# Kernel tuning notes

Measured on AMD Instinct MI355X. Metric: run time of the kernel, lower is better.

## Reference

```python
import jax, jax.numpy as jnp
import numpy as np

B, N, K = 4, 40960, 16
D_IN, D_OUT = 32, 64


def setup_inputs() -> dict:
    key = jax.random.key(0)
    keys = iter(jax.random.split(key, 48))
    def nrm(shape, scale):
        return (jax.random.normal(next(keys), shape, jnp.float32) * scale).astype(jnp.float32)
    inp = {
        "feature": jax.random.normal(next(keys), (B, N, D_IN), jnp.float32),
        "xyz": jax.random.uniform(next(keys), (B, N, 3), jnp.float32),
        "neigh_idx": jax.random.randint(next(keys), (B, N, K), 0, N, jnp.int32),
    }
    def conv_bn(name, cin, cout):
        inp["w_" + name] = nrm((cin, cout), (2.0 / cin) ** 0.5)
        inp["s_" + name] = 1.0 + nrm((cout,), 0.1)  # folded BN scale: gamma/sqrt(var+eps)
        inp["b_" + name] = nrm((cout,), 0.1)        # folded BN bias: beta - mean*scale
    conv_bn("mlp1", D_IN, D_OUT // 2)
    conv_bn("lfa1", 10, D_OUT // 2)
    inp["w_att1_fc"] = nrm((D_OUT, D_OUT), (2.0 / D_OUT) ** 0.5)
    conv_bn("att1_mlp", D_OUT, D_OUT // 2)
    conv_bn("lfa2", D_OUT // 2, D_OUT // 2)
    inp["w_att2_fc"] = nrm((D_OUT, D_OUT), (2.0 / D_OUT) ** 0.5)
    conv_bn("att2_mlp", D_OUT, D_OUT)
    conv_bn("mlp2", D_OUT, 2 * D_OUT)
    conv_bn("sc", D_IN, 2 * D_OUT)
    return inp


def _gather(pc, idx):
    # pc: [B,N,D], idx: [B,N,K] -> [B,N,K,D]
    b, n, k = idx.shape
    flat = jnp.take_along_axis(pc, idx.reshape(b, n * k, 1), axis=1)
    return flat.reshape(b, n, k, pc.shape[-1])


def _cb(x, w, s, b, relu=True):
    # 1x1 conv + folded BN (+ ReLU), channels-last
    y = jnp.einsum('...i,io->...o', x, w) * s + b
    return jnp.maximum(y, 0.0) if relu else y


def _att_pool(fs, w_fc, w, s, b):
    # fs: [B,N,K,C]; softmax-attention pooling over K, then mlp
    scores = jax.nn.softmax(jnp.einsum('bnkc,cd->bnkd', fs, w_fc), axis=2)
    agg = jnp.sum(fs * scores, axis=2)  # [B,N,C]
    return _cb(agg, w, s, b)


def _rel_pos(xyz, idx):
    nbr = _gather(xyz, idx)                           # [B,N,K,3]
    tile = jnp.broadcast_to(xyz[:, :, None, :], nbr.shape)
    rel = tile - nbr
    dist = jnp.sqrt(jnp.sum(rel * rel, axis=-1, keepdims=True))
    return jnp.concatenate([dist, rel, tile, nbr], axis=-1)  # [B,N,K,10]


def reference(feature, xyz, neigh_idx,
              w_mlp1, s_mlp1, b_mlp1,
              w_lfa1, s_lfa1, b_lfa1,
              w_att1_fc, w_att1_mlp, s_att1_mlp, b_att1_mlp,
              w_lfa2, s_lfa2, b_lfa2,
              w_att2_fc, w_att2_mlp, s_att2_mlp, b_att2_mlp,
              w_mlp2, s_mlp2, b_mlp2,
              w_sc, s_sc, b_sc):
    f_pc = _cb(feature, w_mlp1, s_mlp1, b_mlp1)                   # [B,N,d/2]
    f_xyz = _cb(_rel_pos(xyz, neigh_idx), w_lfa1, s_lfa1, b_lfa1)  # [B,N,K,d/2]
    f_nb = _gather(f_pc, neigh_idx)                                # [B,N,K,d/2]
    f_agg = _att_pool(jnp.concatenate([f_nb, f_xyz], axis=-1),
                      w_att1_fc, w_att1_mlp, s_att1_mlp, b_att1_mlp)  # [B,N,d/2]
    f_xyz2 = _cb(f_xyz, w_lfa2, s_lfa2, b_lfa2)                    # [B,N,K,d/2]
    f_nb2 = _gather(f_agg, neigh_idx)                              # [B,N,K,d/2]
    f_pc2 = _att_pool(jnp.concatenate([f_nb2, f_xyz2], axis=-1),
                      w_att2_fc, w_att2_mlp, s_att2_mlp, b_att2_mlp)  # [B,N,d]
    out = _cb(f_pc2, w_mlp2, s_mlp2, b_mlp2, relu=False)           # [B,N,2d]
    sc = _cb(feature, w_sc, s_sc, b_sc, relu=False)
    return jax.nn.leaky_relu(out + sc, negative_slope=0.2)
```

## Files before the change

kernel.cpp:

```cpp
#include <hip/hip_runtime.h>
#include <hip/hip_bf16.h>

#define NPTS  40960
#define BNPTS 163840
#define KNB   16

#define PK_MLP1 0
#define PK_FC1  1280
#define PK_FC2  6912
#define PK_L1   12544
#define PK_L2   13824
#define PK_M1   15104
#define PK_M2   17920
#define PK_W2   23552
#define PK_WS   34816
#define PK_TOTAL 39936

using bf16x8 = __attribute__((ext_vector_type(8))) short;
using f32x4  = __attribute__((ext_vector_type(4))) float;

__device__ __forceinline__ unsigned short f2bf(float x) {
    union { float f; unsigned u; } v; v.f = x;
    unsigned r = v.u + 0x7fffu + ((v.u >> 16) & 1u);
    return (unsigned short)(r >> 16);
}
__device__ __forceinline__ float bf2f(unsigned short u) {
    union { unsigned u; float f; } v; v.u = ((unsigned)u) << 16;
    return v.f;
}
__device__ __forceinline__ unsigned pk2(float lo, float hi) {
    union { __hip_bfloat162 h; unsigned u; } v;
    v.h = __float22bfloat162_rn(float2{lo, hi});
    return v.u;
}
__device__ __forceinline__ bf16x8 pack8(float a0, float a1, float a2, float a3,
                                        float a4, float a5, float a6, float a7) {
    union { unsigned u[4]; bf16x8 v; } w;
    w.u[0] = pk2(a0, a1); w.u[1] = pk2(a2, a3);
    w.u[2] = pk2(a4, a5); w.u[3] = pk2(a6, a7);
    return w.v;
}
__device__ __forceinline__ f32x4 mfma16(bf16x8 a, bf16x8 b, f32x4 c) {
    return __builtin_amdgcn_mfma_f32_16x16x32_bf16(a, b, c, 0, 0, 0);
}
__device__ __forceinline__ float exp2_fast(float x) { return __builtin_amdgcn_exp2f(x); }
__device__ __forceinline__ float rcp_fast(float x)  { return __builtin_amdgcn_rcpf(x); }

__global__ __launch_bounds__(256)
void k_prep(const float* __restrict__ wm1, const float* __restrict__ wfc1,
            const float* __restrict__ wfc2,
            const float* __restrict__ wlfa1, const float* __restrict__ slfa1, const float* __restrict__ blfa1,
            const float* __restrict__ wlfa2,
            const float* __restrict__ wam1, const float* __restrict__ wam2,
            const float* __restrict__ w2, const float* __restrict__ wsc,
            unsigned short* __restrict__ pk)
{
    const int tid = threadIdx.x, blk = blockIdx.x;
    const float LOG2E = 1.4426950408889634f;
    switch (blk) {
    case 0:
        for (int t = tid; t < 32 * 32; t += 256) {
            int c = t >> 5, d = t & 31;
            int slot = (d & 1) * 16 + (d >> 1);
            pk[PK_MLP1 + slot * 40 + c] = f2bf(wm1[t]);
        }
        break;
    case 1:
        for (int t = tid; t < 64 * 64; t += 256) {
            int c = t >> 6, d = t & 63;
            pk[PK_FC1 + d * 88 + c] = f2bf(wfc1[t] * LOG2E);
        }
        break;
    case 2:
        for (int t = tid; t < 64 * 64; t += 256) {
            int c = t >> 6, d = t & 63;
            pk[PK_FC2 + d * 88 + c] = f2bf(wfc2[t] * LOG2E);
        }
        break;
    case 3:
        for (int t = tid; t < 32 * 32; t += 256) {
            int k = t >> 5, d = t & 31;
            int slot = (d & 1) * 16 + (d >> 1);
            float v1 = k < 10 ? wlfa1[k * 32 + d] * slfa1[d] : (k == 10 ? blfa1[d] : 0.f);
            pk[PK_L1 + slot * 40 + k] = f2bf(v1);
            pk[PK_L2 + slot * 40 + k] = f2bf(wlfa2[k * 32 + d]);
        }
        break;
    case 4:
        for (int t = tid; t < 64 * 32; t += 256) {
            int c = t / 32, d = t % 32;
            int slot = (d & 1) * 16 + (d >> 1);
            pk[PK_M1 + slot * 88 + c] = f2bf(wam1[t]);
        }
        break;
    case 5:
        for (int t = tid; t < 64 * 64; t += 256) {
            int c = t >> 6, d = t & 63;
            int slot = (d >> 5) * 32 + (d & 1) * 16 + ((d & 31) >> 1);
            pk[PK_M2 + slot * 88 + c] = f2bf(wam2[t]);
        }
        break;
    case 6:
        for (int t = tid; t < 64 * 128; t += 256) {
            int c = t >> 7, d = t & 127;
            int slot = (d >> 5) * 32 + (d & 1) * 16 + ((d & 31) >> 1);
            pk[PK_W2 + slot * 88 + c] = f2bf(w2[t]);
        }
        break;
    case 7:
        for (int t = tid; t < 32 * 128; t += 256) {
            int c = t >> 7, d = t & 127;
            int slot = (d >> 5) * 32 + (d & 1) * 16 + ((d & 31) >> 1);
            pk[PK_WS + slot * 40 + c] = f2bf(wsc[t]);
        }
        break;
    }
}

__global__ __launch_bounds__(256)
void k_mlp1(const float* __restrict__ feature, const unsigned short* __restrict__ pk,
            const float* __restrict__ s, const float* __restrict__ b,
            unsigned short* __restrict__ f_pc)
{
    const int tid = threadIdx.x;
    const int lid = tid & 63, wv = tid >> 6;
    const int col = lid & 15, quad = lid >> 4;
    bf16x8 B0 = *(const bf16x8*)&pk[PK_MLP1 + col * 40 + quad * 8];
    bf16x8 B1 = *(const bf16x8*)&pk[PK_MLP1 + (16 + col) * 40 + quad * 8];
    float s0 = s[2 * col], b0 = b[2 * col], s1 = s[2 * col + 1], b1 = b[2 * col + 1];
    for (int itp = 0; itp < 4; itp++) {
        const int p0 = blockIdx.x * 256 + wv * 64 + itp * 16;
        const float* fr = &feature[(size_t)(p0 + col) * 32 + quad * 8];
        float4 u0 = *(const float4*)fr;
        float4 u1 = *(const float4*)(fr + 4);
        bf16x8 a = pack8(u0.x, u0.y, u0.z, u0.w, u1.x, u1.y, u1.z, u1.w);
        f32x4 z = {0.f, 0.f, 0.f, 0.f};
        f32x4 d0 = mfma16(a, B0, z);
        f32x4 d1 = mfma16(a, B1, z);
        #pragma unroll
        for (int r = 0; r < 4; r++) {
            int p = p0 + quad * 4 + r;
            float ye = fmaxf(d0[r] * s0 + b0, 0.f);
            float yo = fmaxf(d1[r] * s1 + b1, 0.f);
            *(unsigned*)&f_pc[(size_t)p * 32 + 2 * col] = pk2(ye, yo);
        }
    }
}

template<int NOUT, bool HAS_LFA2>
__global__ __launch_bounds__(256, 4)
void k_att(const float* __restrict__ xyz, const int* __restrict__ nidx,
           const unsigned short* __restrict__ src,
           const unsigned short* __restrict__ wl1T, const unsigned short* __restrict__ wl2T,
           const float* __restrict__ slfa2, const float* __restrict__ blfa2,
           const unsigned short* __restrict__ wfcT, const unsigned short* __restrict__ wmT,
           const float* __restrict__ smlp, const float* __restrict__ bmlp,
           unsigned short* __restrict__ out)
{
    constexpr int NP = NOUT / 32;
    constexpr int WS = 88;
    __shared__ __align__(16) char smem[27648];
    char* uni = smem;

    const int tid = threadIdx.x;
    const int lid = tid & 63, wv = tid >> 6;
    const int col = lid & 15, quad = lid >> 4;

    bf16x8 Bfc[4][2];
    #pragma unroll
    for (int nt = 0; nt < 4; nt++)
        #pragma unroll
        for (int ks = 0; ks < 2; ks++)
            Bfc[nt][ks] = *(const bf16x8*)&wfcT[(nt * 16 + col) * WS + ks * 32 + quad * 8];
    bf16x8 Bl1e = *(const bf16x8*)&wl1T[col * 40 + quad * 8];
    bf16x8 Bl1o = *(const bf16x8*)&wl1T[(16 + col) * 40 + quad * 8];
    bf16x8 Bl2e{}, Bl2o{};
    float sl2e = 0.f, bl2e = 0.f, sl2o = 0.f, bl2o = 0.f;
    if (HAS_LFA2) {
        Bl2e = *(const bf16x8*)&wl2T[col * 40 + quad * 8];
        Bl2o = *(const bf16x8*)&wl2T[(16 + col) * 40 + quad * 8];
        sl2e = slfa2[2 * col]; bl2e = blfa2[2 * col];
        sl2o = slfa2[2 * col + 1]; bl2o = blfa2[2 * col + 1];
    }
    float sme[NP], bme[NP], smo[NP], bmo[NP];
    #pragma unroll
    for (int tp = 0; tp < NP; tp++) {
        sme[tp] = smlp[tp * 32 + 2 * col]; bme[tp] = bmlp[tp * 32 + 2 * col];
        smo[tp] = smlp[tp * 32 + 2 * col + 1]; bmo[tp] = bmlp[tp * 32 + 2 * col + 1];
    }
    bf16x8 Bme_r[2], Bmo_r[2];
    if constexpr (NOUT == 32) {
        #pragma unroll
        for (int ks = 0; ks < 2; ks++) {
            Bme_r[ks] = *(const bf16x8*)&wmT[col * WS + ks * 32 + quad * 8];
            Bmo_r[ks] = *(const bf16x8*)&wmT[(16 + col) * WS + ks * 32 + quad * 8];
        }
    }

    unsigned short* fc  = (unsigned short*)(uni) + wv * 2816;
    unsigned short* ag  = (unsigned short*)(uni + 22528) + wv * 288;
    unsigned short* nb  = (unsigned short*)(uni + 24832) + wv * 256;
    float*          cxy = (float*)(uni + 26880) + wv * 48;

    const int blk = (int)blockIdx.x;
    const int vblk = (blk & 7) * 320 + (blk >> 3);
    const int pbase = vblk * 64 + wv * 16;
    const int pb = (pbase / NPTS) * NPTS;
    const unsigned short* srcb = src + (size_t)pb * 32;
    const float* xyzb = xyz + (size_t)pb * 3;

    {
        int4 t4 = *(const int4*)&nidx[(size_t)pbase * KNB + lid * 4];
        ushort4 u = make_ushort4((unsigned short)t4.x, (unsigned short)t4.y,
                                 (unsigned short)t4.z, (unsigned short)t4.w);
        *(ushort4*)&nb[lid * 4] = u;
        if (lid < 48) cxy[lid] = xyz[(size_t)pbase * 3 + lid];
    }

    const f32x4 z = {0.f, 0.f, 0.f, 0.f};
    bf16x8 vs; float nx = 0.f, ny = 0.f, nz = 0.f;
    {
        int j = (int)nb[col];
        vs = *(const bf16x8*)(srcb + (size_t)j * 32 + quad * 8);
        if (quad < 2) { const float* xp = xyzb + (size_t)j * 3; nx = xp[0]; ny = xp[1]; nz = xp[2]; }
    }

    #pragma unroll 2
    for (int it = 0; it < 16; it++) {
        const int p = pbase + it;
        unsigned short* fcb = fc + (it & 1) * 1408;
        bf16x8 a0 = vs;
        *(bf16x8*)&fcb[col * WS + quad * 8] = a0;

        float cx = cxy[it * 3], cy = cxy[it * 3 + 1], cz = cxy[it * 3 + 2];
        float rx = cx - nx, ry = cy - ny, rz = cz - nz;
        float dd = sqrtf(rx * rx + ry * ry + rz * rz);
        float f0 = 0.f, f1 = 0.f, f2 = 0.f, f3 = 0.f, f4 = 0.f, f5 = 0.f, f6 = 0.f, f7 = 0.f;
        if (quad == 0)      { f0 = dd; f1 = rx; f2 = ry; f3 = rz; f4 = cx; f5 = cy; f6 = cz; f7 = nx; }
        else if (quad == 1) { f0 = ny; f1 = nz; f2 = 1.0f; }
        bf16x8 al = pack8(f0, f1, f2, f3, f4, f5, f6, f7);

        {
            int itn = it < 15 ? it + 1 : 15;
            int j = (int)nb[itn * 16 + col];
            vs = *(const bf16x8*)(srcb + (size_t)j * 32 + quad * 8);
            if (quad < 2) { const float* xp = xyzb + (size_t)j * 3; nx = xp[0]; ny = xp[1]; nz = xp[2]; }
        }

        {
            f32x4 d0 = mfma16(al, Bl1e, z);
            f32x4 d1 = mfma16(al, Bl1o, z);
            #pragma unroll
            for (int r = 0; r < 4; r++) {
                float ye = fmaxf(d0[r], 0.f);
                float yo = fmaxf(d1[r], 0.f);
                *(unsigned*)&fcb[(quad * 4 + r) * WS + 32 + 2 * col] = pk2(ye, yo);
            }
            if (HAS_LFA2) {
                bf16x8 a2 = *(const bf16x8*)&fcb[col * WS + 32 + quad * 8];
                f32x4 e0 = mfma16(a2, Bl2e, z);
                f32x4 e1 = mfma16(a2, Bl2o, z);
                #pragma unroll
                for (int r = 0; r < 4; r++) {
                    float ye = fmaxf(e0[r] * sl2e + bl2e, 0.f);
                    float yo = fmaxf(e1[r] * sl2o + bl2o, 0.f);
                    *(unsigned*)&fcb[(quad * 4 + r) * WS + 32 + 2 * col] = pk2(ye, yo);
                }
            }
        }

        {
            bf16x8 a1 = *(const bf16x8*)&fcb[col * WS + 32 + quad * 8];
            #pragma unroll
            for (int nt = 0; nt < 4; nt++) {
                f32x4 L = mfma16(a1, Bfc[nt][1], mfma16(a0, Bfc[nt][0], z));
                float e0 = exp2_fast(L[0]), e1 = exp2_fast(L[1]);
                float e2 = exp2_fast(L[2]), e3 = exp2_fast(L[3]);
                float sden = (e0 + e1) + (e2 + e3);
                const unsigned short* frr = &fcb[quad * 4 * WS + nt * 16 + col];
                float av = e0 * bf2f(frr[0]) + e1 * bf2f(frr[WS]) + e2 * bf2f(frr[2 * WS]) + e3 * bf2f(frr[3 * WS]);
                av   += __shfl_xor(av, 16, 64);
                sden += __shfl_xor(sden, 16, 64);
                av   += __shfl_xor(av, 32, 64);
                sden += __shfl_xor(sden, 32, 64);
                if (quad == 0) ag[(it & 3) * 72 + nt * 16 + col] = f2bf(av * rcp_fast(sden));
            }
        }

        if ((it & 3) == 3) {
            bf16x8 am0 = *(const bf16x8*)&ag[(col & 3) * 72 + quad * 8];
            bf16x8 am1 = *(const bf16x8*)&ag[(col & 3) * 72 + 32 + quad * 8];
            #pragma unroll
            for (int tp = 0; tp < NP; tp++) {
                bf16x8 Be0, Be1, Bo0, Bo1;
                if constexpr (NOUT == 32) {
                    Be0 = Bme_r[0]; Be1 = Bme_r[1];
                    Bo0 = Bmo_r[0]; Bo1 = Bmo_r[1];
                } else {
                    Be0 = *(const bf16x8*)&wmT[(tp * 32 + col) * WS + quad * 8];
                    Be1 = *(const bf16x8*)&wmT[(tp * 32 + col) * WS + 32 + quad * 8];
                    Bo0 = *(const bf16x8*)&wmT[(tp * 32 + 16 + col) * WS + quad * 8];
                    Bo1 = *(const bf16x8*)&wmT[(tp * 32 + 16 + col) * WS + 32 + quad * 8];
                }
                f32x4 de = mfma16(am1, Be1, mfma16(am0, Be0, z));
                f32x4 dq = mfma16(am1, Bo1, mfma16(am0, Bo0, z));
                if (quad == 0) {
                    #pragma unroll
                    for (int r = 0; r < 4; r++) {
                        float ye = fmaxf(de[r] * sme[tp] + bme[tp], 0.f);
                        float yo = fmaxf(dq[r] * smo[tp] + bmo[tp], 0.f);
                        *(unsigned*)&out[(size_t)(p - 3 + r) * NOUT + tp * 32 + 2 * col] = pk2(ye, yo);
                    }
                }
            }
        }
    }
}

__global__ __launch_bounds__(256)
void k_out(const unsigned short* __restrict__ f_pc2, const float* __restrict__ feature,
           const unsigned short* __restrict__ pk,
           const float* __restrict__ s2, const float* __restrict__ b2,
           const float* __restrict__ ssc, const float* __restrict__ bsc,
           float* __restrict__ out)
{
    const int tid = threadIdx.x;
    const int lid = tid & 63, wv = tid >> 6;
    const int col = lid & 15, quad = lid >> 4;
    const unsigned short* w2T = pk + PK_W2;
    const unsigned short* wsT = pk + PK_WS;
    float sse[4], sso[4], ste[4], sto[4], bbe[4], bbo[4];
    #pragma unroll
    for (int m = 0; m < 4; m++) {
        int ce = m * 32 + 2 * col, co = ce + 1;
        sse[m] = s2[ce]; sso[m] = s2[co];
        ste[m] = ssc[ce]; sto[m] = ssc[co];
        bbe[m] = b2[ce] + bsc[ce]; bbo[m] = b2[co] + bsc[co];
    }
    const f32x4 z = {0.f, 0.f, 0.f, 0.f};
    #pragma unroll 1
    for (int itp = 0; itp < 2; itp++) {
        const int p0 = blockIdx.x * 128 + wv * 32 + itp * 16;
        const unsigned short* ar = &f_pc2[(size_t)(p0 + col) * 64 + quad * 8];
        bf16x8 a10 = *(const bf16x8*)ar;
        bf16x8 a11 = *(const bf16x8*)(ar + 32);
        const float* fr = &feature[(size_t)(p0 + col) * 32 + quad * 8];
        float4 u0 = *(const float4*)fr;
        float4 u1 = *(const float4*)(fr + 4);
        bf16x8 a2 = pack8(u0.x, u0.y, u0.z, u0.w, u1.x, u1.y, u1.z, u1.w);
        #pragma unroll
        for (int m = 0; m < 4; m++) {
            bf16x8 ke0 = *(const bf16x8*)&w2T[(m * 32 + col) * 88 + quad * 8];
            bf16x8 ke1 = *(const bf16x8*)&w2T[(m * 32 + col) * 88 + 32 + quad * 8];
            bf16x8 ko0 = *(const bf16x8*)&w2T[(m * 32 + 16 + col) * 88 + quad * 8];
            bf16x8 ko1 = *(const bf16x8*)&w2T[(m * 32 + 16 + col) * 88 + 32 + quad * 8];
            bf16x8 se  = *(const bf16x8*)&wsT[(m * 32 + col) * 40 + quad * 8];
            bf16x8 so  = *(const bf16x8*)&wsT[(m * 32 + 16 + col) * 40 + quad * 8];
            f32x4 de = mfma16(a11, ke1, mfma16(a10, ke0, z));
            f32x4 dq = mfma16(a11, ko1, mfma16(a10, ko0, z));
            f32x4 ee = mfma16(a2, se, z);
            f32x4 eo = mfma16(a2, so, z);
            #pragma unroll
            for (int r = 0; r < 4; r++) {
                float ye = de[r] * sse[m] + ee[r] * ste[m] + bbe[m];
                float yo = dq[r] * sso[m] + eo[r] * sto[m] + bbo[m];
                ye = ye > 0.f ? ye : 0.2f * ye;
                yo = yo > 0.f ? yo : 0.2f * yo;
                *(float2*)&out[(size_t)(p0 + quad * 4 + r) * 128 + m * 32 + 2 * col] =
                    make_float2(ye, yo);
            }
        }
    }
}

extern "C" void kernel_launch(void* const* d_in, const int* in_sizes, int n_in,
                              void* d_out, int out_size, void* d_ws, size_t ws_size,
                              hipStream_t stream) {
    const float* feature = (const float*)d_in[0];
    const float* xyz     = (const float*)d_in[1];
    const int*   nidx    = (const int*)d_in[2];
    const float* w_mlp1 = (const float*)d_in[3];
    const float* s_mlp1 = (const float*)d_in[4];
    const float* b_mlp1 = (const float*)d_in[5];
    const float* w_lfa1 = (const float*)d_in[6];
    const float* s_lfa1 = (const float*)d_in[7];
    const float* b_lfa1 = (const float*)d_in[8];
    const float* w_att1_fc  = (const float*)d_in[9];
    const float* w_att1_mlp = (const float*)d_in[10];
    const float* s_att1_mlp = (const float*)d_in[11];
    const float* b_att1_mlp = (const float*)d_in[12];
    const float* w_lfa2 = (const float*)d_in[13];
    const float* s_lfa2 = (const float*)d_in[14];
    const float* b_lfa2 = (const float*)d_in[15];
    const float* w_att2_fc  = (const float*)d_in[16];
    const float* w_att2_mlp = (const float*)d_in[17];
    const float* s_att2_mlp = (const float*)d_in[18];
    const float* b_att2_mlp = (const float*)d_in[19];
    const float* w_mlp2 = (const float*)d_in[20];
    const float* s_mlp2 = (const float*)d_in[21];
    const float* b_mlp2 = (const float*)d_in[22];
    const float* w_sc = (const float*)d_in[23];
    const float* s_sc = (const float*)d_in[24];
    const float* b_sc = (const float*)d_in[25];

    unsigned short* f_pc  = (unsigned short*)d_ws;
    unsigned short* f_agg = f_pc  + (size_t)BNPTS * 32;
    unsigned short* f_pc2 = f_agg + (size_t)BNPTS * 32;
    unsigned short* pkw   = f_pc2 + (size_t)BNPTS * 64;
    float* out = (float*)d_out;

    k_prep<<<8, 256, 0, stream>>>(w_mlp1, w_att1_fc, w_att2_fc,
                                  w_lfa1, s_lfa1, b_lfa1, w_lfa2,
                                  w_att1_mlp, w_att2_mlp, w_mlp2, w_sc, pkw);
    k_mlp1<<<BNPTS / 256, 256, 0, stream>>>(feature, pkw, s_mlp1, b_mlp1, f_pc);
    k_att<32, false><<<BNPTS / 64, 256, 0, stream>>>(
        xyz, nidx, f_pc,
        pkw + PK_L1, pkw + PK_L1,
        s_lfa1, b_lfa1,
        pkw + PK_FC1, pkw + PK_M1, s_att1_mlp, b_att1_mlp, f_agg);
    k_att<64, true><<<BNPTS / 64, 256, 0, stream>>>(
        xyz, nidx, f_agg,
        pkw + PK_L1, pkw + PK_L2,
        s_lfa2, b_lfa2,
        pkw + PK_FC2, pkw + PK_M2, s_att2_mlp, b_att2_mlp, f_pc2);
    k_out<<<BNPTS / 128, 256, 0, stream>>>(
        f_pc2, feature, pkw,
        s_mlp2, b_mlp2, s_sc, b_sc, out);
}
```

Before: 365.5 us.

## Pad xyz to float4 for gathers and batch attention-MLP epilogue per wave

Adds a prep pass that repacks xyz into a padded float4 array, so each neighbor coordinate gather in the attention kernels becomes a single 16-byte load instead of three scalar loads. The attention kernels also drop the double-buffered feature tile and the every-4-points MLP epilogue. They now collect all 16 aggregated rows in shared memory and run one 16-row MFMA epilogue per wave, with all lanes storing output. This reduces shared memory and per-iteration branching, at the cost of extra xyz4 workspace, an extra prep pass, and a fully serial loop (unroll 1) with less overlap across iterations.

```diff
diff --git a/kernel.cpp b/kernel.cpp
--- a/kernel.cpp
+++ b/kernel.cpp
@@ -53,10 +53,17 @@
             const float* __restrict__ wlfa2,
             const float* __restrict__ wam1, const float* __restrict__ wam2,
             const float* __restrict__ w2, const float* __restrict__ wsc,
-            unsigned short* __restrict__ pk)
+            const float* __restrict__ xyz,
+            unsigned short* __restrict__ pk, float* __restrict__ xyz4)
 {
     const int tid = threadIdx.x, blk = blockIdx.x;
     const float LOG2E = 1.4426950408889634f;
+    if (blk >= 8) {
+        int idx = (blk - 8) * 256 + tid;
+        float3 v = *(const float3*)&xyz[(size_t)idx * 3];
+        *(float4*)&xyz4[(size_t)idx * 4] = make_float4(v.x, v.y, v.z, 0.f);
+        return;
+    }
     switch (blk) {
     case 0:
         for (int t = tid; t < 32 * 32; t += 256) {
@@ -149,7 +156,7 @@
 
 template<int NOUT, bool HAS_LFA2>
 __global__ __launch_bounds__(256, 4)
-void k_att(const float* __restrict__ xyz, const int* __restrict__ nidx,
+void k_att(const float* __restrict__ xyz4, const int* __restrict__ nidx,
            const unsigned short* __restrict__ src,
            const unsigned short* __restrict__ wl1T, const unsigned short* __restrict__ wl2T,
            const float* __restrict__ slfa2, const float* __restrict__ blfa2,
@@ -159,7 +166,7 @@
 {
     constexpr int NP = NOUT / 32;
     constexpr int WS = 88;
-    __shared__ __align__(16) char smem[27648];
+    __shared__ __align__(16) char smem[23552];
     char* uni = smem;
 
     const int tid = threadIdx.x;
@@ -188,33 +195,26 @@
         sme[tp] = smlp[tp * 32 + 2 * col]; bme[tp] = bmlp[tp * 32 + 2 * col];
         smo[tp] = smlp[tp * 32 + 2 * col + 1]; bmo[tp] = bmlp[tp * 32 + 2 * col + 1];
     }
-    bf16x8 Bme_r[2], Bmo_r[2];
-    if constexpr (NOUT == 32) {
-        #pragma unroll
-        for (int ks = 0; ks < 2; ks++) {
-            Bme_r[ks] = *(const bf16x8*)&wmT[col * WS + ks * 32 + quad * 8];
-            Bmo_r[ks] = *(const bf16x8*)&wmT[(16 + col) * WS + ks * 32 + quad * 8];
-        }
-    }
-
-    unsigned short* fc  = (unsigned short*)(uni) + wv * 2816;
-    unsigned short* ag  = (unsigned short*)(uni + 22528) + wv * 288;
-    unsigned short* nb  = (unsigned short*)(uni + 24832) + wv * 256;
-    float*          cxy = (float*)(uni + 26880) + wv * 48;
+
+    unsigned short* fc  = (unsigned short*)(uni) + wv * 1408;
+    unsigned short* ag  = (unsigned short*)(uni + 11264) + wv * 1152;
+    unsigned short* nb  = (unsigned short*)(uni + 20480) + wv * 256;
+    float*          cxy = (float*)(uni + 22528) + wv * 64;
 
     const int blk = (int)blockIdx.x;
     const int vblk = (blk & 7) * 320 + (blk >> 3);
     const int pbase = vblk * 64 + wv * 16;
     const int pb = (pbase / NPTS) * NPTS;
     const unsigned short* srcb = src + (size_t)pb * 32;
-    const float* xyzb = xyz + (size_t)pb * 3;
+    const float4* x4  = (const float4*)xyz4;
+    const float4* x4b = x4 + pb;
 
     {
         int4 t4 = *(const int4*)&nidx[(size_t)pbase * KNB + lid * 4];
         ushort4 u = make_ushort4((unsigned short)t4.x, (unsigned short)t4.y,
                                  (unsigned short)t4.z, (unsigned short)t4.w);
         *(ushort4*)&nb[lid * 4] = u;
-        if (lid < 48) cxy[lid] = xyz[(size_t)pbase * 3 + lid];
+        if (lid < 16) *(float4*)&cxy[lid * 4] = x4[pbase + lid];
     }
 
     const f32x4 z = {0.f, 0.f, 0.f, 0.f};
@@ -222,17 +222,15 @@
     {
         int j = (int)nb[col];
         vs = *(const bf16x8*)(srcb + (size_t)j * 32 + quad * 8);
-        if (quad < 2) { const float* xp = xyzb + (size_t)j * 3; nx = xp[0]; ny = xp[1]; nz = xp[2]; }
-    }
-
-    #pragma unroll 2
+        if (quad < 2) { float4 t = x4b[j]; nx = t.x; ny = t.y; nz = t.z; }
+    }
+
+    #pragma unroll 1
     for (int it = 0; it < 16; it++) {
-        const int p = pbase + it;
-        unsigned short* fcb = fc + (it & 1) * 1408;
         bf16x8 a0 = vs;
-        *(bf16x8*)&fcb[col * WS + quad * 8] = a0;
-
-        float cx = cxy[it * 3], cy = cxy[it * 3 + 1], cz = cxy[it * 3 + 2];
+        *(bf16x8*)&fc[col * WS + quad * 8] = a0;
+
+        float cx = cxy[it * 4], cy = cxy[it * 4 + 1], cz = cxy[it * 4 + 2];
         float rx = cx - nx, ry = cy - ny, rz = cz - nz;
         float dd = sqrtf(rx * rx + ry * ry + rz * rz);
         float f0 = 0.f, f1 = 0.f, f2 = 0.f, f3 = 0.f, f4 = 0.f, f5 = 0.f, f6 = 0.f, f7 = 0.f;
@@ -244,7 +242,7 @@
             int itn = it < 15 ? it + 1 : 15;
             int j = (int)nb[itn * 16 + col];
             vs = *(const bf16x8*)(srcb + (size_t)j * 32 + quad * 8);
-            if (quad < 2) { const float* xp = xyzb + (size_t)j * 3; nx = xp[0]; ny = xp[1]; nz = xp[2]; }
+            if (quad < 2) { float4 t = x4b[j]; nx = t.x; ny = t.y; nz = t.z; }
         }
 
         {
@@ -254,64 +252,65 @@
             for (int r = 0; r < 4; r++) {
                 float ye = fmaxf(d0[r], 0.f);
                 float yo = fmaxf(d1[r], 0.f);
-                *(unsigned*)&fcb[(quad * 4 + r) * WS + 32 + 2 * col] = pk2(ye, yo);
+                *(unsigned*)&fc[(quad * 4 + r) * WS + 32 + 2 * col] = pk2(ye, yo);
             }
             if (HAS_LFA2) {
-                bf16x8 a2 = *(const bf16x8*)&fcb[col * WS + 32 + quad * 8];
+                bf16x8 a2 = *(const bf16x8*)&fc[col * WS + 32 + quad * 8];
                 f32x4 e0 = mfma16(a2, Bl2e, z);
                 f32x4 e1 = mfma16(a2, Bl2o, z);
                 #pragma unroll
                 for (int r = 0; r < 4; r++) {
                     float ye = fmaxf(e0[r] * sl2e + bl2e, 0.f);
                     float yo = fmaxf(e1[r] * sl2o + bl2o, 0.f);
-                    *(unsigned*)&fcb[(quad * 4 + r) * WS + 32 + 2 * col] = pk2(ye, yo);
+                    *(unsigned*)&fc[(quad * 4 + r) * WS + 32 + 2 * col] = pk2(ye, yo);
                 }
             }
         }
 
         {
-            bf16x8 a1 = *(const bf16x8*)&fcb[col * WS + 32 + quad * 8];
+            bf16x8 a1 = *(const bf16x8*)&fc[col * WS + 32 + quad * 8];
             #pragma unroll
             for (int nt = 0; nt < 4; nt++) {
                 f32x4 L = mfma16(a1, Bfc[nt][1], mfma16(a0, Bfc[nt][0], z));
                 float e0 = exp2_fast(L[0]), e1 = exp2_fast(L[1]);
                 float e2 = exp2_fast(L[2]), e3 = exp2_fast(L[3]);
                 float sden = (e0 + e1) + (e2 + e3);
-                const unsigned short* frr = &fcb[quad * 4 * WS + nt * 16 + col];
+                const unsigned short* frr = &fc[quad * 4 * WS + nt * 16 + col];
                 float av = e0 * bf2f(frr[0]) + e1 * bf2f(frr[WS]) + e2 * bf2f(frr[2 * WS]) + e3 * bf2f(frr[3 * WS]);
                 av   += __shfl_xor(av, 16, 64);
                 sden += __shfl_xor(sden, 16, 64);
                 av   += __shfl_xor(av, 32, 64);
                 sden += __shfl_xor(sden, 32, 64);
-                if (quad == 0) ag[(it & 3) * 72 + nt * 16 + col] = f2bf(av * rcp_fast(sden));
-            }
-        }
-
-        if ((it & 3) == 3) {
-            bf16x8 am0 = *(const bf16x8*)&ag[(col & 3) * 72 + quad * 8];
-            bf16x8 am1 = *(const bf16x8*)&ag[(col & 3) * 72 + 32 + quad * 8];
+                if (quad == 0) ag[it * 72 + nt * 16 + col] = f2bf(av * rcp_fast(sden));
+            }
+        }
+    }
+
+    {
+        bf16x8 am0 = *(const bf16x8*)&ag[col * 72 + quad * 8];
+        bf16x8 am1 = *(const bf16x8*)&ag[col * 72 + 32 + quad * 8];
+        #pragma unroll
+        for (int tp = 0; tp < NP; tp++) {
+            bf16x8 Be0, Be1, Bo0, Bo1;
+            if constexpr (NOUT == 32) {
+                Be0 = *(const bf16x8*)&wmT[col * WS + quad * 8];
+                Be1 = *(const bf16x8*)&wmT[col * WS + 32 + quad * 8];
+                Bo0 = *(const bf16x8*)&wmT[(16 + col) * WS + quad * 8];
+                Bo1 = *(const bf16x8*)&wmT[(16 + col) * WS + 32 + quad * 8];
+            } else {
+                Be0 = *(const bf16x8*)&wmT[(tp * 32 + col) * WS + quad * 8];
+                Be1 = *(const bf16x8*)&wmT[(tp * 32 + col) * WS + 32 + quad * 8];
+                Bo0 = *(const bf16x8*)&wmT[(tp * 32 + 16 + col) * WS + quad * 8];
+                Bo1 = *(const bf16x8*)&wmT[(tp * 32 + 16 + col) * WS + 32 + quad * 8];
+            }
+            f32x4 de = mfma16(am1, Be1, mfma16(am0, Be0, z));
+            f32x4 dq = mfma16(am1, Bo1, mfma16(am0, Bo0, z));
             #pragma unroll
-            for (int tp = 0; tp < NP; tp++) {
-                bf16x8 Be0, Be1, Bo0, Bo1;
-                if constexpr (NOUT == 32) {
-                    Be0 = Bme_r[0]; Be1 = Bme_r[1];
-                    Bo0 = Bmo_r[0]; Bo1 = Bmo_r[1];
-                } else {
-                    Be0 = *(const bf16x8*)&wmT[(tp * 32 + col) * WS + quad * 8];
-                    Be1 = *(const bf16x8*)&wmT[(tp * 32 + col) * WS + 32 + quad * 8];
-                    Bo0 = *(const bf16x8*)&wmT[(tp * 32 + 16 + col) * WS + quad * 8];
-                    Bo1 = *(const bf16x8*)&wmT[(tp * 32 + 16 + col) * WS + 32 + quad * 8];
-                }
-                f32x4 de = mfma16(am1, Be1, mfma16(am0, Be0, z));
-                f32x4 dq = mfma16(am1, Bo1, mfma16(am0, Bo0, z));
-                if (quad == 0) {
-                    #pragma unroll
-                    for (int r = 0; r < 4; r++) {
-                        float ye = fmaxf(de[r] * sme[tp] + bme[tp], 0.f);
-                        float yo = fmaxf(dq[r] * smo[tp] + bmo[tp], 0.f);
-                        *(unsigned*)&out[(size_t)(p - 3 + r) * NOUT + tp * 32 + 2 * col] = pk2(ye, yo);
-                    }
-                }
+            for (int r = 0; r < 4; r++) {
+                int pp = pbase + quad * 4 + r;
+                float ye = fmaxf(de[r] * sme[tp] + bme[tp], 0.f);
+                float yo = fmaxf(dq[r] * smo[tp] + bmo[tp], 0.f);
+                *(unsigned*)&out[(size_t)pp * NOUT + tp * 32 + 2 * col] = pk2(ye, yo);
             }
         }
     }
@@ -407,19 +406,21 @@
     unsigned short* f_agg = f_pc  + (size_t)BNPTS * 32;
     unsigned short* f_pc2 = f_agg + (size_t)BNPTS * 32;
     unsigned short* pkw   = f_pc2 + (size_t)BNPTS * 64;
+    float*          xyz4  = (float*)(pkw + PK_TOTAL);
     float* out = (float*)d_out;
 
-    k_prep<<<8, 256, 0, stream>>>(w_mlp1, w_att1_fc, w_att2_fc,
-                                  w_lfa1, s_lfa1, b_lfa1, w_lfa2,
-                                  w_att1_mlp, w_att2_mlp, w_mlp2, w_sc, pkw);
+    k_prep<<<8 + BNPTS / 256, 256, 0, stream>>>(
+        w_mlp1, w_att1_fc, w_att2_fc,
+        w_lfa1, s_lfa1, b_lfa1, w_lfa2,
+        w_att1_mlp, w_att2_mlp, w_mlp2, w_sc, xyz, pkw, xyz4);
     k_mlp1<<<BNPTS / 256, 256, 0, stream>>>(feature, pkw, s_mlp1, b_mlp1, f_pc);
     k_att<32, false><<<BNPTS / 64, 256, 0, stream>>>(
-        xyz, nidx, f_pc,
+        xyz4, nidx, f_pc,
         pkw + PK_L1, pkw + PK_L1,
         s_lfa1, b_lfa1,
         pkw + PK_FC1, pkw + PK_M1, s_att1_mlp, b_att1_mlp, f_agg);
     k_att<64, true><<<BNPTS / 64, 256, 0, stream>>>(
-        xyz, nidx, f_agg,
+        xyz4, nidx, f_agg,
         pkw + PK_L1, pkw + PK_L2,
         s_lfa2, b_lfa2,
         pkw + PK_FC2, pkw + PK_M2, s_att2_mlp, b_att2_mlp, f_pc2);
```

New measurement: 351.0 us. -4.0%, faster.
